# Kernel tuning notes

Hardware: AMD Instinct MI355X
Metric: run time of the kernel (lower is better)

## Reference

```python
import jax, jax.numpy as jnp
import numpy as np
import math

H = 8  # num_heads
# mock_theta_f Taylor coefficients: K(q) = 1 + q - 2q^2 + 3q^3
COEFFS = (1.0, 1.0, -2.0, 3.0)


def setup_inputs() -> dict:
    key = jax.random.key(0)
    ks = jax.random.split(key, 12)
    B, L, E = 2, 2048, 512
    s = 0.02
    return {
        "query": jax.random.normal(ks[0], (B, L, E), jnp.float32),
        "key_": jax.random.normal(ks[1], (B, L, E), jnp.float32),
        "value": jax.random.normal(ks[2], (B, L, E), jnp.float32),
        "Wq": jax.random.normal(ks[3], (E, E), jnp.float32) * s,
        "bq": jnp.zeros((E,), jnp.float32),
        "Wk": jax.random.normal(ks[4], (E, E), jnp.float32) * s,
        "bk": jnp.zeros((E,), jnp.float32),
        "Wv": jax.random.normal(ks[5], (E, E), jnp.float32) * s,
        "bv": jnp.zeros((E,), jnp.float32),
        "Wo": jax.random.normal(ks[6], (E, E), jnp.float32) * s,
        "bo": jnp.zeros((E,), jnp.float32),
        "log_tau": jnp.zeros((), jnp.float32),  # tau = exp(0) = 1.0
    }


def _horner(q):
    a0, a1, a2, a3 = COEFFS
    val = jnp.full_like(q, a3)
    val = q * val + a2
    val = q * val + a1
    val = q * val + a0
    return jnp.maximum(val, 0.0)


def _attn(query, key_, value, Wq, bq, Wk, bk, Wv, bv, Wo, bo, log_tau):
    B, L, E = query.shape
    S = key_.shape[1]
    Hd = E // H
    scale = math.sqrt(Hd)

    Q = (query @ Wq.T + bq).reshape(B, L, H, Hd).transpose(0, 2, 1, 3)  # (B,H,L,Hd)
    K = (key_ @ Wk.T + bk).reshape(B, S, H, Hd).transpose(0, 2, 1, 3)
    V = (value @ Wv.T + bv).reshape(B, S, H, Hd).transpose(0, 2, 1, 3)

    scores = jnp.einsum("bhld,bhsd->bhls", Q, K) / scale  # (B,H,L,S)

    tau = jnp.exp(log_tau)
    q = jax.nn.sigmoid(scores / tau)
    kv = _horner(q)

    # causal mask (is_causal=True): mask strict upper triangle
    causal = jnp.triu(jnp.ones((L, S), dtype=bool), k=1)  # (L,S)
    kv = jnp.where(causal[None, None], 0.0, kv)

    denom = jnp.sum(kv, axis=-1, keepdims=True)
    weights = kv / jnp.maximum(denom, 1e-12)

    out = jnp.einsum("bhls,bhsd->bhld", weights, V)  # (B,H,L,Hd)
    out = out.transpose(0, 2, 1, 3).reshape(B, L, E)
    return out @ Wo.T + bo


def reference(query, key_, value, Wq, bq, Wk, bk, Wv, bv, Wo, bo, log_tau):
    return _attn(query, key_, value, Wq, bq, Wk, bk, Wv, bv, Wo, bo, log_tau)
```

## Files before the change

kernel.cpp:

```cpp
#include <hip/hip_runtime.h>
#include <hip/hip_bf16.h>


typedef __attribute__((ext_vector_type(8))) __bf16 bf16x8;
typedef __attribute__((ext_vector_type(4))) __bf16 bf16x4;
typedef __attribute__((ext_vector_type(4))) float f32x4;

#define NB 2
#define NL 2048
#define NE 512
#define NH 8
#define HD 64
#define NROW (NB * NL)
#define NJOB 144

__device__ __forceinline__ void gload16(const void* g, void* l) {
  __builtin_amdgcn_global_load_lds(
      (const __attribute__((address_space(1))) void*)g,
      (__attribute__((address_space(3))) void*)l, 16, 0, 0);
}

__global__ __launch_bounds__(256) void cvt_qkv(
    const float* __restrict__ q, const float* __restrict__ k,
    const float* __restrict__ v, __bf16* __restrict__ qo,
    __bf16* __restrict__ ko, __bf16* __restrict__ vo) {
  const int gid = blockIdx.x * 256 + threadIdx.x;
  const int seg = gid >> 19;
  const int i = gid & ((1 << 19) - 1);
  const float* s = seg == 0 ? q : (seg == 1 ? k : v);
  __bf16* d = seg == 0 ? qo : (seg == 1 ? ko : vo);
  float4 x = ((const float4*)s)[i];
  bf16x4 o = {(__bf16)x.x, (__bf16)x.y, (__bf16)x.z, (__bf16)x.w};
  ((bf16x4*)d)[i] = o;
}

__global__ __launch_bounds__(256) void cvt_w(
    const float* __restrict__ w0, const float* __restrict__ w1,
    const float* __restrict__ w2, const float* __restrict__ w3,
    __bf16* __restrict__ o0, __bf16* __restrict__ o1,
    __bf16* __restrict__ o2, __bf16* __restrict__ o3) {
  const int gid = blockIdx.x * 256 + threadIdx.x;
  const int seg = gid >> 16;
  const int i = gid & 0xFFFF;
  const float* s = seg == 0 ? w0 : (seg == 1 ? w1 : (seg == 2 ? w2 : w3));
  __bf16* d = seg == 0 ? o0 : (seg == 1 ? o1 : (seg == 2 ? o2 : o3));
  float4 x = ((const float4*)s)[i];
  bf16x4 o = {(__bf16)x.x, (__bf16)x.y, (__bf16)x.z, (__bf16)x.w};
  ((bf16x4*)d)[i] = o;
}

template <int MODE>
__device__ __forceinline__ void gemm_body(const __bf16* __restrict__ A,
                                          const __bf16* __restrict__ W,
                                          const float* __restrict__ bias,
                                          __bf16* __restrict__ outb,
                                          float* __restrict__ outf) {
  __shared__ __align__(16) __bf16 As[128 * 32];
  __shared__ __align__(16) __bf16 Ws[128 * 32];

  const int tid = threadIdx.x;
  const int lane = tid & 63, w = tid >> 6;
  const int lr = lane & 15, lg = lane >> 4;
  const int brow = blockIdx.y * 128, bcol = blockIdx.x * 128;
  const int wr = (w >> 1) * 64, wc = (w & 1) * 64;

  f32x4 zero4 = {0.f, 0.f, 0.f, 0.f};
  f32x4 acc[4][4];
#pragma unroll
  for (int i = 0; i < 4; ++i)
#pragma unroll
    for (int j = 0; j < 4; ++j) acc[i][j] = zero4;

  const int c0 = tid, c1 = tid + 256;
  const int r0 = c0 >> 2, cc0 = c0 & 3;
  const int r1 = c1 >> 2, cc1 = c1 & 3;

  for (int k0 = 0; k0 < NE; k0 += 32) {
    __syncthreads();
    gload16(A + (size_t)(brow + r0) * NE + k0 + cc0 * 8, As + c0 * 8);
    gload16(W + (size_t)(bcol + r0) * NE + k0 + cc0 * 8, Ws + c0 * 8);
    gload16(A + (size_t)(brow + r1) * NE + k0 + cc1 * 8, As + c1 * 8);
    gload16(W + (size_t)(bcol + r1) * NE + k0 + cc1 * 8, Ws + c1 * 8);
    __syncthreads();

    bf16x8 af[4], wf[4];
#pragma unroll
    for (int mi = 0; mi < 4; ++mi)
      af[mi] = *(const bf16x8*)(As + (wr + mi * 16 + lr) * 32 + lg * 8);
#pragma unroll
    for (int ni = 0; ni < 4; ++ni)
      wf[ni] = *(const bf16x8*)(Ws + (wc + ni * 16 + lr) * 32 + lg * 8);
#pragma unroll
    for (int mi = 0; mi < 4; ++mi)
#pragma unroll
      for (int ni = 0; ni < 4; ++ni)
        acc[mi][ni] = __builtin_amdgcn_mfma_f32_16x16x32_bf16(
            af[mi], wf[ni], acc[mi][ni], 0, 0, 0);
  }

#pragma unroll
  for (int mi = 0; mi < 4; ++mi) {
#pragma unroll
    for (int ni = 0; ni < 4; ++ni) {
      const int col = bcol + wc + ni * 16 + lr;
      const float bv = bias[col];
#pragma unroll
      for (int r = 0; r < 4; ++r) {
        const int row = brow + wr + mi * 16 + lg * 4 + r;
        const float v = acc[mi][ni][r] + bv;
        if (MODE == 0) {
          const int b = row >> 11, l = row & (NL - 1);
          const int h = col >> 6, d = col & 63;
          outb[(((size_t)b * NH + h) * NL + l) * HD + d] = (__bf16)v;
        } else if (MODE == 2) {
          const int b = row >> 11, l = row & (NL - 1);
          const int h = col >> 6, d = col & 63;
          outb[(((size_t)b * NH + h) * HD + d) * NL + l] = (__bf16)v;
        } else {
          outf[(size_t)row * NE + col] = v;
        }
      }
    }
  }
}

__global__ __launch_bounds__(256) void qkv_gemm(
    const __bf16* __restrict__ A0, const __bf16* __restrict__ A1,
    const __bf16* __restrict__ A2, const __bf16* __restrict__ W0,
    const __bf16* __restrict__ W1, const __bf16* __restrict__ W2,
    const float* __restrict__ b0, const float* __restrict__ b1,
    const float* __restrict__ b2, __bf16* __restrict__ O0,
    __bf16* __restrict__ O1, __bf16* __restrict__ O2) {
  const int z = blockIdx.z;
  if (z == 2) {
    gemm_body<2>(A2, W2, b2, O2, nullptr);
  } else {
    const __bf16* A = z == 0 ? A0 : A1;
    const __bf16* W = z == 0 ? W0 : W1;
    const float* bias = z == 0 ? b0 : b1;
    __bf16* O = z == 0 ? O0 : O1;
    gemm_body<0>(A, W, bias, O, nullptr);
  }
}

__global__ __launch_bounds__(256) void out_gemm(const __bf16* __restrict__ A,
                                                const __bf16* __restrict__ W,
                                                const float* __restrict__ bias,
                                                float* __restrict__ outf) {
  gemm_body<1>(A, W, bias, nullptr, outf);
}

template <int SLOTTED>
__global__ __launch_bounds__(256) void attn_kernel(
    const __bf16* __restrict__ Qg, const __bf16* __restrict__ Kg,
    const __bf16* __restrict__ VTg, float* __restrict__ numg,
    float* __restrict__ deng, const float* __restrict__ log_tau) {
  __shared__ __align__(16) __bf16 Kt[64][72];
  __shared__ __align__(16) __bf16 Vt[64][72];
  __shared__ __align__(16) __bf16 Pl[4][16][72];

  const int j = blockIdx.x;
  int qb, c;
  if (j < 32) {
    c = 0; qb = j;
  } else if (j < 60) {
    c = 1; qb = j - 28;
  } else if (j < 84) {
    c = 2; qb = j - 52;
  } else if (j < 104) {
    c = 3; qb = j - 72;
  } else if (j < 120) {
    c = 4; qb = j - 88;
  } else if (j < 132) {
    c = 5; qb = j - 100;
  } else if (j < 140) {
    c = 6; qb = j - 108;
  } else {
    c = 7; qb = j - 112;
  }
  const int bh = blockIdx.y;
  const __bf16* Qh = Qg + (size_t)bh * NL * HD;
  const __bf16* Kh = Kg + (size_t)bh * NL * HD;
  const __bf16* Vth = VTg + (size_t)bh * HD * NL;

  const int tid = threadIdx.x;
  const int lane = tid & 63, w = tid >> 6;
  const int lr = lane & 15, lg = lane >> 4;
  const float ninv = -1.44269504f / (8.0f * __expf(log_tau[0]));

  const int q0 = qb * 64;
  const int qrow = q0 + w * 16 + lr;
  bf16x8 qf[2];
  qf[0] = *(const bf16x8*)(Qh + (size_t)qrow * HD + lg * 8);
  qf[1] = *(const bf16x8*)(Qh + (size_t)qrow * HD + 32 + lg * 8);

  f32x4 zero4 = {0.f, 0.f, 0.f, 0.f};
  f32x4 o_acc[4];
#pragma unroll
  for (int n = 0; n < 4; ++n) o_acc[n] = zero4;
  float den[4] = {0.f, 0.f, 0.f, 0.f};

  const int t0 = c * 4;
  const int t1 = min(t0 + 4, qb + 1);

  const int kr0 = tid >> 3, kc0 = (tid & 7) * 8;

  bf16x8 kpa = *(const bf16x8*)(Kh + (size_t)(t0 * 64 + kr0) * HD + kc0);
  bf16x8 kpb = *(const bf16x8*)(Kh + (size_t)(t0 * 64 + kr0 + 32) * HD + kc0);
  bf16x8 vpa = *(const bf16x8*)(Vth + (size_t)kr0 * NL + t0 * 64 + kc0);
  bf16x8 vpb = *(const bf16x8*)(Vth + (size_t)(kr0 + 32) * NL + t0 * 64 + kc0);

  for (int t = t0; t < t1; ++t) {
    const int kv0 = t * 64;
    __syncthreads();
    *(bf16x8*)&Kt[kr0][kc0] = kpa;
    *(bf16x8*)&Kt[kr0 + 32][kc0] = kpb;
    *(bf16x8*)&Vt[kr0][kc0] = vpa;
    *(bf16x8*)&Vt[kr0 + 32][kc0] = vpb;
    __syncthreads();

    if (t + 1 < t1) {
      const int kn = (t + 1) * 64;
      kpa = *(const bf16x8*)(Kh + (size_t)(kn + kr0) * HD + kc0);
      kpb = *(const bf16x8*)(Kh + (size_t)(kn + kr0 + 32) * HD + kc0);
      vpa = *(const bf16x8*)(Vth + (size_t)kr0 * NL + kn + kc0);
      vpb = *(const bf16x8*)(Vth + (size_t)(kr0 + 32) * NL + kn + kc0);
    }

    f32x4 sacc[4];
#pragma unroll
    for (int si = 0; si < 4; ++si) sacc[si] = zero4;
#pragma unroll
    for (int kk = 0; kk < 2; ++kk) {
#pragma unroll
      for (int si = 0; si < 4; ++si) {
        bf16x8 kf = *(const bf16x8*)&Kt[si * 16 + lr][kk * 32 + lg * 8];
        sacc[si] = __builtin_amdgcn_mfma_f32_16x16x32_bf16(qf[kk], kf,
                                                           sacc[si], 0, 0, 0);
      }
    }

#pragma unroll
    for (int si = 0; si < 4; ++si) {
      const int sg = kv0 + si * 16 + lr;
#pragma unroll
      for (int r = 0; r < 4; ++r) {
        const int qg = q0 + w * 16 + lg * 4 + r;
        const float e = __builtin_amdgcn_exp2f(sacc[si][r] * ninv);
        const float qs = __builtin_amdgcn_rcpf(1.0f + e);
        float kvv = fmaf(qs, fmaf(qs, fmaf(qs, 3.0f, -2.0f), 1.0f), 1.0f);
        kvv = fmaxf(kvv, 0.0f);
        if (sg > qg) kvv = 0.0f;
        const __bf16 kb = (__bf16)kvv;
        Pl[w][lg * 4 + r][si * 16 + lr] = kb;
        sacc[si][r] = (float)kb;
      }
    }

#pragma unroll
    for (int r = 0; r < 4; ++r) {
      float rsv = sacc[0][r] + sacc[1][r] + sacc[2][r] + sacc[3][r];
#pragma unroll
      for (int m = 1; m < 16; m <<= 1) rsv += __shfl_xor(rsv, m, 64);
      den[r] += rsv;
    }

#pragma unroll
    for (int kk = 0; kk < 2; ++kk) {
      bf16x8 pf = *(const bf16x8*)&Pl[w][lr][kk * 32 + lg * 8];
#pragma unroll
      for (int n = 0; n < 4; ++n) {
        bf16x8 vf = *(const bf16x8*)&Vt[n * 16 + lr][kk * 32 + lg * 8];
        o_acc[n] = __builtin_amdgcn_mfma_f32_16x16x32_bf16(pf, vf, o_acc[n],
                                                           0, 0, 0);
      }
    }
  }

  if (SLOTTED) {
    float* nslot = numg + (((size_t)bh * NJOB + j) << 12);
    const int lrow = w * 16 + lg * 4;
    if (lr == 0) {
      float* dslot = deng + (((size_t)bh * NJOB + j) << 6);
#pragma unroll
      for (int r = 0; r < 4; ++r) dslot[lrow + r] = den[r];
    }
#pragma unroll
    for (int n = 0; n < 4; ++n) {
      const int col = n * 16 + lr;
#pragma unroll
      for (int r = 0; r < 4; ++r) nslot[(lrow + r) * 64 + col] = o_acc[n][r];
    }
  } else {
    const int orow = q0 + w * 16 + lg * 4;
    if (lr == 0) {
#pragma unroll
      for (int r = 0; r < 4; ++r)
        atomicAdd(&deng[(size_t)bh * NL + orow + r], den[r]);
    }
#pragma unroll
    for (int n = 0; n < 4; ++n) {
      const int col = n * 16 + lr;
#pragma unroll
      for (int r = 0; r < 4; ++r)
        atomicAdd(&numg[((size_t)bh * NL + orow + r) * HD + col], o_acc[n][r]);
    }
  }
}

__global__ __launch_bounds__(256) void combine_slotted(
    const float* __restrict__ numS, const float* __restrict__ denS,
    __bf16* __restrict__ AO) {
  const int gid = blockIdx.x * 256 + threadIdx.x;
  const int d4 = gid & 15;
  const int row = gid >> 4;
  const int bh = row >> 11, l = row & (NL - 1);
  const int b = bh >> 3, h = bh & 7;
  const int qb = l >> 6, lrow = l & 63;
  const int nc = (qb >> 2) + 1;

  f32x4 acc = {0.f, 0.f, 0.f, 0.f};
  float d = 0.f;
  for (int c = 0; c < nc; ++c) {
    const int jj = qb + 2 * c * (15 - c);
    const size_t sb = (size_t)bh * NJOB + jj;
    acc += *(const f32x4*)(numS + ((sb << 6) + lrow) * 64 + d4 * 4);
    d += denS[(sb << 6) + lrow];
  }
  const float idv = __builtin_amdgcn_rcpf(fmaxf(d, 1e-12f));
  bf16x4 o = {(__bf16)(acc[0] * idv), (__bf16)(acc[1] * idv),
              (__bf16)(acc[2] * idv), (__bf16)(acc[3] * idv)};
  *(bf16x4*)&AO[((size_t)b * NL + l) * NE + h * HD + d4 * 4] = o;
}

__global__ __launch_bounds__(256) void combine_kernel(
    const float* __restrict__ numg, const float* __restrict__ deng,
    __bf16* __restrict__ AO) {
  const int gid = blockIdx.x * 256 + threadIdx.x;
  const int d4 = gid & 15;
  const int row = gid >> 4;
  const int bh = row >> 11, l = row & (NL - 1);
  const int b = bh >> 3, h = bh & 7;
  f32x4 n4 = ((const f32x4*)numg)[gid];
  const float idv = __builtin_amdgcn_rcpf(fmaxf(deng[row], 1e-12f));
  bf16x4 o = {(__bf16)(n4[0] * idv), (__bf16)(n4[1] * idv),
              (__bf16)(n4[2] * idv), (__bf16)(n4[3] * idv)};
  *(bf16x4*)&AO[((size_t)b * NL + l) * NE + h * HD + d4 * 4] = o;
}

extern "C" void kernel_launch(void* const* d_in, const int* in_sizes, int n_in,
                              void* d_out, int out_size, void* d_ws,
                              size_t ws_size, hipStream_t stream) {
  const float* query = (const float*)d_in[0];
  const float* key_ = (const float*)d_in[1];
  const float* value = (const float*)d_in[2];
  const float* Wq = (const float*)d_in[3];
  const float* bq = (const float*)d_in[4];
  const float* Wk = (const float*)d_in[5];
  const float* bk = (const float*)d_in[6];
  const float* Wv = (const float*)d_in[7];
  const float* bv = (const float*)d_in[8];
  const float* Wo = (const float*)d_in[9];
  const float* bo = (const float*)d_in[10];
  const float* log_tau = (const float*)d_in[11];

  char* ws = (char*)d_ws;
  const size_t MB = 1024 * 1024;
  const bool slotted = (ws_size >= 55 * MB);

  __bf16* xb = (__bf16*)(ws + 0 * MB);
  __bf16* kxb = (__bf16*)(ws + 4 * MB);
  __bf16* vxb = (__bf16*)(ws + 8 * MB);

  __bf16 *wqb, *wkb, *wvb, *wob, *Qh, *Kh, *VT, *AO;
  float *numb, *denb;
  if (slotted) {
    numb = (float*)(ws + 0 * MB);
    denb = (float*)(ws + 36 * MB);
    wqb = (__bf16*)(ws + 37 * MB);
    wkb = (__bf16*)(ws + 37 * MB + 512 * 1024);
    wvb = (__bf16*)(ws + 38 * MB);
    wob = (__bf16*)(ws + 38 * MB + 512 * 1024);
    Qh = (__bf16*)(ws + 39 * MB);
    Kh = (__bf16*)(ws + 43 * MB);
    VT = (__bf16*)(ws + 47 * MB);
    AO = (__bf16*)(ws + 51 * MB);
  } else {
    numb = (float*)(ws + 0 * MB);
    denb = (float*)(ws + 8 * MB);
    wqb = (__bf16*)(ws + 12 * MB);
    wkb = (__bf16*)(ws + 12 * MB + 512 * 1024);
    wvb = (__bf16*)(ws + 13 * MB);
    wob = (__bf16*)(ws + 13 * MB + 512 * 1024);
    Qh = (__bf16*)(ws + 14 * MB);
    Kh = (__bf16*)(ws + 18 * MB);
    VT = (__bf16*)(ws + 22 * MB);
    AO = (__bf16*)(ws + 26 * MB);
  }

  cvt_qkv<<<3 * (1 << 19) / 256, 256, 0, stream>>>(query, key_, value, xb, kxb,
                                                   vxb);
  cvt_w<<<4 * (1 << 16) / 256, 256, 0, stream>>>(Wq, Wk, Wv, Wo, wqb, wkb, wvb,
                                                 wob);

  dim3 gq(NE / 128, NROW / 128, 3);
  qkv_gemm<<<gq, 256, 0, stream>>>(xb, kxb, vxb, wqb, wkb, wvb, bq, bk, bv, Qh,
                                   Kh, VT);

  dim3 ga(NJOB, NB * NH);
  if (slotted) {
    attn_kernel<1><<<ga, 256, 0, stream>>>(Qh, Kh, VT, numb, denb, log_tau);
    combine_slotted<<<2048, 256, 0, stream>>>(numb, denb, AO);
  } else {
    hipMemsetAsync(ws, 0, 8 * MB + 128 * 1024, stream);
    attn_kernel<0><<<ga, 256, 0, stream>>>(Qh, Kh, VT, numb, denb, log_tau);
    combine_kernel<<<2048, 256, 0, stream>>>(numb, denb, AO);
  }

  dim3 gg(NE / 128, NROW / 128);
  out_gemm<<<gg, 256, 0, stream>>>(AO, wob, bo, (float*)d_out);
}
```

Before: 82.24 us.

## Compute transposed scores and pass probabilities via ds_bpermute instead of LDS

Swaps the MFMA operands so the score tile comes out transposed, with each lane holding one query row. The probabilities are packed into bf16 pairs and redistributed into the PV MFMA operand layout with ds_bpermute, replacing the per-wave LDS staging buffer. The row-sum denominator is now accumulated per lane and needs only two cross-lane shuffles at the end instead of a 16-wide shuffle reduction every tile. The fmax clamp is dropped on the grounds that the polynomial is positive for inputs in (0,1). In exchange it adds eight bpermutes and some select logic per tile.

```diff
diff --git a/kernel.cpp b/kernel.cpp
--- a/kernel.cpp
+++ b/kernel.cpp
@@ -5,6 +5,7 @@
 typedef __attribute__((ext_vector_type(8))) __bf16 bf16x8;
 typedef __attribute__((ext_vector_type(4))) __bf16 bf16x4;
 typedef __attribute__((ext_vector_type(4))) float f32x4;
+typedef __attribute__((ext_vector_type(4))) int i32x4;
 
 #define NB 2
 #define NL 2048
@@ -157,7 +158,6 @@
     float* __restrict__ deng, const float* __restrict__ log_tau) {
   __shared__ __align__(16) __bf16 Kt[64][72];
   __shared__ __align__(16) __bf16 Vt[64][72];
-  __shared__ __align__(16) __bf16 Pl[4][16][72];
 
   const int j = blockIdx.x;
   int qb, c;
@@ -189,16 +189,16 @@
   const float ninv = -1.44269504f / (8.0f * __expf(log_tau[0]));
 
   const int q0 = qb * 64;
-  const int qrow = q0 + w * 16 + lr;
+  const int qg = q0 + w * 16 + lr;
   bf16x8 qf[2];
-  qf[0] = *(const bf16x8*)(Qh + (size_t)qrow * HD + lg * 8);
-  qf[1] = *(const bf16x8*)(Qh + (size_t)qrow * HD + 32 + lg * 8);
+  qf[0] = *(const bf16x8*)(Qh + (size_t)qg * HD + lg * 8);
+  qf[1] = *(const bf16x8*)(Qh + (size_t)qg * HD + 32 + lg * 8);
 
   f32x4 zero4 = {0.f, 0.f, 0.f, 0.f};
   f32x4 o_acc[4];
 #pragma unroll
   for (int n = 0; n < 4; ++n) o_acc[n] = zero4;
-  float den[4] = {0.f, 0.f, 0.f, 0.f};
+  float den_l = 0.f;
 
   const int t0 = c * 4;
   const int t1 = min(t0 + 4, qb + 1);
@@ -209,6 +209,9 @@
   bf16x8 kpb = *(const bf16x8*)(Kh + (size_t)(t0 * 64 + kr0 + 32) * HD + kc0);
   bf16x8 vpa = *(const bf16x8*)(Vth + (size_t)kr0 * NL + t0 * 64 + kc0);
   bf16x8 vpb = *(const bf16x8*)(Vth + (size_t)(kr0 + 32) * NL + t0 * 64 + kc0);
+
+  const int idxA = (((lane & 16) << 1) + lr) * 4;
+  const bool hi = (lane & 32) != 0;
 
   for (int t = t0; t < t1; ++t) {
     const int kv0 = t * 64;
@@ -235,39 +238,43 @@
 #pragma unroll
       for (int si = 0; si < 4; ++si) {
         bf16x8 kf = *(const bf16x8*)&Kt[si * 16 + lr][kk * 32 + lg * 8];
-        sacc[si] = __builtin_amdgcn_mfma_f32_16x16x32_bf16(qf[kk], kf,
+        sacc[si] = __builtin_amdgcn_mfma_f32_16x16x32_bf16(kf, qf[kk],
                                                            sacc[si], 0, 0, 0);
       }
     }
 
+    unsigned pk[4][2];
 #pragma unroll
     for (int si = 0; si < 4; ++si) {
-      const int sg = kv0 + si * 16 + lr;
+      const int sb = kv0 + si * 16 + lg * 4;
+      unsigned kbv[4];
 #pragma unroll
       for (int r = 0; r < 4; ++r) {
-        const int qg = q0 + w * 16 + lg * 4 + r;
         const float e = __builtin_amdgcn_exp2f(sacc[si][r] * ninv);
         const float qs = __builtin_amdgcn_rcpf(1.0f + e);
         float kvv = fmaf(qs, fmaf(qs, fmaf(qs, 3.0f, -2.0f), 1.0f), 1.0f);
-        kvv = fmaxf(kvv, 0.0f);
-        if (sg > qg) kvv = 0.0f;
+        if (sb + r > qg) kvv = 0.0f;
         const __bf16 kb = (__bf16)kvv;
-        Pl[w][lg * 4 + r][si * 16 + lr] = kb;
-        sacc[si][r] = (float)kb;
+        den_l += (float)kb;
+        kbv[r] = (unsigned)__builtin_bit_cast(unsigned short, kb);
       }
-    }
-
-#pragma unroll
-    for (int r = 0; r < 4; ++r) {
-      float rsv = sacc[0][r] + sacc[1][r] + sacc[2][r] + sacc[3][r];
-#pragma unroll
-      for (int m = 1; m < 16; m <<= 1) rsv += __shfl_xor(rsv, m, 64);
-      den[r] += rsv;
+      pk[si][0] = kbv[0] | (kbv[1] << 16);
+      pk[si][1] = kbv[2] | (kbv[3] << 16);
     }
 
 #pragma unroll
     for (int kk = 0; kk < 2; ++kk) {
-      bf16x8 pf = *(const bf16x8*)&Pl[w][lr][kk * 32 + lg * 8];
+      const int sl = kk * 2, sh = kk * 2 + 1;
+      const int a0 = __builtin_amdgcn_ds_bpermute(idxA, (int)pk[sl][0]);
+      const int a1 = __builtin_amdgcn_ds_bpermute(idxA, (int)pk[sl][1]);
+      const int b0 = __builtin_amdgcn_ds_bpermute(idxA + 64, (int)pk[sl][0]);
+      const int b1 = __builtin_amdgcn_ds_bpermute(idxA + 64, (int)pk[sl][1]);
+      const int c0 = __builtin_amdgcn_ds_bpermute(idxA, (int)pk[sh][0]);
+      const int c1 = __builtin_amdgcn_ds_bpermute(idxA, (int)pk[sh][1]);
+      const int d0 = __builtin_amdgcn_ds_bpermute(idxA + 64, (int)pk[sh][0]);
+      const int d1 = __builtin_amdgcn_ds_bpermute(idxA + 64, (int)pk[sh][1]);
+      i32x4 pw = {hi ? c0 : a0, hi ? c1 : a1, hi ? d0 : b0, hi ? d1 : b1};
+      bf16x8 pf = __builtin_bit_cast(bf16x8, pw);
 #pragma unroll
       for (int n = 0; n < 4; ++n) {
         bf16x8 vf = *(const bf16x8*)&Vt[n * 16 + lr][kk * 32 + lg * 8];
@@ -277,13 +284,15 @@
     }
   }
 
+  den_l += __shfl_xor(den_l, 16, 64);
+  den_l += __shfl_xor(den_l, 32, 64);
+
   if (SLOTTED) {
     float* nslot = numg + (((size_t)bh * NJOB + j) << 12);
     const int lrow = w * 16 + lg * 4;
-    if (lr == 0) {
+    if (lg == 0) {
       float* dslot = deng + (((size_t)bh * NJOB + j) << 6);
-#pragma unroll
-      for (int r = 0; r < 4; ++r) dslot[lrow + r] = den[r];
+      dslot[w * 16 + lr] = den_l;
     }
 #pragma unroll
     for (int n = 0; n < 4; ++n) {
@@ -293,11 +302,7 @@
     }
   } else {
     const int orow = q0 + w * 16 + lg * 4;
-    if (lr == 0) {
-#pragma unroll
-      for (int r = 0; r < 4; ++r)
-        atomicAdd(&deng[(size_t)bh * NL + orow + r], den[r]);
-    }
+    if (lg == 0) atomicAdd(&deng[(size_t)bh * NL + q0 + w * 16 + lr], den_l);
 #pragma unroll
     for (int n = 0; n < 4; ++n) {
       const int col = n * 16 + lr;
```

After: 79.57 us. 3.2% less time.
